# Optimization experiments

Measured on AMD Instinct MI355X. Metric: run time of the kernel, lower is better.

## Reference

```python
import jax, jax.numpy as jnp
import numpy as np

N = 100000   # nodes
E = 1600000  # edges (avg degree 16)
H = 4        # heads
D = 32       # per-head dim (= output_dim)
IN = 32      # input_dim (== output_dim for residual)
NEG_SLOPE = 0.2  # DGL GATConv leaky_relu default


def setup_inputs() -> dict:
    key = jax.random.key(0)
    ks = jax.random.split(key, 9)
    h = jax.random.normal(ks[0], (N, IN), jnp.float32)
    src = jax.random.randint(ks[1], (E,), 0, N, jnp.int32)
    dst = jax.random.randint(ks[2], (E,), 0, N, jnp.int32)
    W_fc = jax.random.normal(ks[3], (IN, H * D), jnp.float32) / np.sqrt(IN).astype(np.float32)
    attn_l = jax.random.normal(ks[4], (H, D), jnp.float32) * 0.1
    attn_r = jax.random.normal(ks[5], (H, D), jnp.float32) * 0.1
    bias_gat = jnp.zeros((H * D,), jnp.float32)
    W_out = jax.random.normal(ks[6], (H * D, D), jnp.float32) / np.sqrt(H * D).astype(np.float32)
    b_out = jnp.zeros((D,), jnp.float32)
    return {"h": h, "src": src, "dst": dst, "W_fc": W_fc, "attn_l": attn_l,
            "attn_r": attn_r, "bias_gat": bias_gat, "W_out": W_out, "b_out": b_out}


def reference(h, src, dst, W_fc, attn_l, attn_r, bias_gat, W_out, b_out):
    # GATConv: linear projection to [N, H, D]
    feat = (h @ W_fc).reshape(N, H, D)
    el = jnp.einsum('nhd,hd->nh', feat, attn_l)  # [N,H]
    er = jnp.einsum('nhd,hd->nh', feat, attn_r)  # [N,H]
    # per-edge unnormalized score, leaky relu
    e = el[src] + er[dst]                         # [E,H]
    e = jnp.where(e > 0, e, NEG_SLOPE * e)
    # segment softmax over edges grouped by destination node
    emax = jax.ops.segment_max(e, dst, num_segments=N)            # [N,H]
    ex = jnp.exp(e - emax[dst])                                   # [E,H]
    denom = jax.ops.segment_sum(ex, dst, num_segments=N)         # [N,H]
    alpha = ex / jnp.maximum(denom[dst], 1e-9)                    # [E,H]
    # attention-weighted scatter-add aggregation
    msg = feat[src] * alpha[:, :, None]                           # [E,H,D]
    rst = jax.ops.segment_sum(msg, dst, num_segments=N)          # [N,H,D]
    rst = rst.reshape(N, H * D) + bias_gat
    # out projection + ELU activation + residual
    out = rst @ W_out + b_out
    out = jnp.where(out > 0, out, jnp.expm1(out))  # ELU(alpha=1)
    return h + out
```

## Files before the change

### kernel.cpp

```cpp
#include <hip/hip_runtime.h>
#include <hip/hip_bf16.h>

#define NNODE 100000
#define NEDGE 1600000
#define NBLK_SCAN 98
#define KPH_BLOCKS 1564
#define FLAGBIT 0x80000000u

static __device__ __forceinline__ uint32_t pack_bf16(float a, float b) {
    __hip_bfloat162 t = __float22bfloat162_rn(make_float2(a, b));
    return *(uint32_t*)&t;
}

__global__ __launch_bounds__(256) void k_proj_hist(
        const float* __restrict__ hin, const float* __restrict__ Wfc,
        const float* __restrict__ attn_l, const float* __restrict__ attn_r,
        uint32_t* __restrict__ feat, float* __restrict__ el, float* __restrict__ er,
        const int* __restrict__ dst, int* __restrict__ cnt, int* __restrict__ pos) {
    int tid = threadIdx.x;
    int ei = blockIdx.x * 256 + tid;
    bool have = ei < NEDGE / 4;
    int4 d, p;
    if (have) {
        d = ((const int4*)dst)[ei];
        p.x = atomicAdd(&cnt[d.x], 1);
        p.y = atomicAdd(&cnt[d.y], 1);
        p.z = atomicAdd(&cnt[d.z], 1);
        p.w = atomicAdd(&cnt[d.w], 1);
    }
    int l = tid & 63;
    int w = tid >> 6;
    int nbase = blockIdx.x * 64 + w * 16;
    int c0 = l * 2;
    float2 wreg[32];
#pragma unroll
    for (int k = 0; k < 32; k++)
        wreg[k] = *(const float2*)&Wfc[k * 128 + c0];
    float al0 = attn_l[c0], al1 = attn_l[c0 + 1];
    float ar0 = attn_r[c0], ar1 = attn_r[c0 + 1];
#pragma unroll 4
    for (int i = 0; i < 16; i++) {
        int n = nbase + i;
        if (n >= NNODE) break;
        float4 hv[8];
#pragma unroll
        for (int j = 0; j < 8; j++)
            hv[j] = *(const float4*)&hin[n * 32 + j * 4];
        float a0 = 0.f, a1 = 0.f;
#pragma unroll
        for (int j = 0; j < 8; j++) {
            a0 = fmaf(hv[j].x, wreg[j * 4 + 0].x, a0); a1 = fmaf(hv[j].x, wreg[j * 4 + 0].y, a1);
            a0 = fmaf(hv[j].y, wreg[j * 4 + 1].x, a0); a1 = fmaf(hv[j].y, wreg[j * 4 + 1].y, a1);
            a0 = fmaf(hv[j].z, wreg[j * 4 + 2].x, a0); a1 = fmaf(hv[j].z, wreg[j * 4 + 2].y, a1);
            a0 = fmaf(hv[j].w, wreg[j * 4 + 3].x, a0); a1 = fmaf(hv[j].w, wreg[j * 4 + 3].y, a1);
        }
        float ep = a0 * al0 + a1 * al1;
        float rp = a0 * ar0 + a1 * ar1;
#pragma unroll
        for (int m = 8; m; m >>= 1) {
            ep += __shfl_xor(ep, m);
            rp += __shfl_xor(rp, m);
        }
        if ((l & 15) == 0) {
            el[n * 4 + (l >> 4)] = ep;
            er[n * 4 + (l >> 4)] = rp;
        }
        feat[(size_t)n * 64 + l] = pack_bf16(a0, a1);
    }
    if (have) ((int4*)pos)[ei] = p;
}

__global__ __launch_bounds__(256) void k_scan(
        const int* __restrict__ cnt, unsigned* __restrict__ word,
        int* __restrict__ offa) {
    __shared__ int s[256];
    __shared__ int sBase;
    int t = threadIdx.x;
    int b = blockIdx.x;
    int base = b * 1024 + t * 4;
    int v[4];
#pragma unroll
    for (int i = 0; i < 4; i++) {
        int n = base + i;
        v[i] = (n < NNODE) ? cnt[n] : 0;
    }
    int sum = v[0] + v[1] + v[2] + v[3];
    s[t] = sum;
    __syncthreads();
    for (int d = 1; d < 256; d <<= 1) {
        int x = (t >= d) ? s[t - d] : 0;
        __syncthreads();
        s[t] += x;
        __syncthreads();
    }
    int excl = s[t] - sum;
    if (t == 255)
        __hip_atomic_store(&word[b], (unsigned)s[255] | FLAGBIT,
                           __ATOMIC_RELEASE, __HIP_MEMORY_SCOPE_AGENT);
    if (t < 64) {
        unsigned acc = 0;
        for (int i = t; i < b; i += 64) {
            unsigned wv;
            do {
                wv = __hip_atomic_load(&word[i], __ATOMIC_ACQUIRE, __HIP_MEMORY_SCOPE_AGENT);
            } while (!(wv & FLAGBIT));
            acc += wv & ~FLAGBIT;
        }
#pragma unroll
        for (int o = 32; o; o >>= 1) acc += __shfl_down(acc, o);
        if (t == 0) sBase = (int)acc;
    }
    __syncthreads();
    int o0 = sBase + excl;
#pragma unroll
    for (int i = 0; i < 4; i++) {
        int n = base + i;
        if (n < NNODE) { offa[n] = o0; o0 += v[i]; }
    }
    if (b == NBLK_SCAN - 1 && t == 255) offa[NNODE] = NEDGE;
}

__global__ __launch_bounds__(256) void k_scatter(const int* __restrict__ src,
                                                 const int* __restrict__ dst,
                                                 const int* __restrict__ pos,
                                                 const int* __restrict__ offa,
                                                 int* __restrict__ ssrc) {
    int i = blockIdx.x * 256 + threadIdx.x;
    if (i >= NEDGE / 4) return;
    int4 s = ((const int4*)src)[i];
    int4 d = ((const int4*)dst)[i];
    int4 p = ((const int4*)pos)[i];
    int o0 = offa[d.x];
    int o1 = offa[d.y];
    int o2 = offa[d.z];
    int o3 = offa[d.w];
    ssrc[o0 + p.x] = s.x;
    ssrc[o1 + p.y] = s.y;
    ssrc[o2 + p.z] = s.z;
    ssrc[o3 + p.w] = s.w;
}

#define NPB 4
union SmemU {
    struct { int sS[NPB][64]; float sE[NPB][64][4]; } g;
    struct { float sv[NPB][128]; float sacc[NPB][2][32]; } e;
};

__global__ __launch_bounds__(256) void k_gather(
        const int* __restrict__ off, const int* __restrict__ ssrc,
        const float* __restrict__ el, const float* __restrict__ er,
        const uint32_t* __restrict__ feat, const float* __restrict__ bias_gat,
        const float* __restrict__ Wout, const float* __restrict__ b_out,
        const float* __restrict__ hin, float* __restrict__ out) {
    __shared__ float sW[128 * 32];
    __shared__ __align__(16) SmemU U;
    int tid = threadIdx.x;
    for (int i = tid * 4; i < 4096; i += 1024)
        *(float4*)&sW[i] = *(const float4*)&Wout[i];
    int w = tid >> 6;
    int l = tid & 63;
    int n = blockIdx.x * NPB + w;
    int c0 = l * 2;
    int hh = l >> 4;
    float2 acc = make_float2(0.f, 0.f);
    float den = 0.f;
    int beg = off[n], end = off[n + 1];
    float4 erv = *(const float4*)&er[n * 4];

    for (int base = beg; base < end; base += 64) {
        int cnt = end - base; if (cnt > 64) cnt = 64;
        int s = 0;
        float4 e4 = make_float4(0.f, 0.f, 0.f, 0.f);
        if (l < cnt) {
            s = ssrc[base + l];
            float4 ev = *(const float4*)&el[s * 4];
            e4.x = ev.x + erv.x; e4.x = e4.x > 0.f ? e4.x : 0.2f * e4.x; e4.x = __expf(e4.x);
            e4.y = ev.y + erv.y; e4.y = e4.y > 0.f ? e4.y : 0.2f * e4.y; e4.y = __expf(e4.y);
            e4.z = ev.z + erv.z; e4.z = e4.z > 0.f ? e4.z : 0.2f * e4.z; e4.z = __expf(e4.z);
            e4.w = ev.w + erv.w; e4.w = e4.w > 0.f ? e4.w : 0.2f * e4.w; e4.w = __expf(e4.w);
        }
        U.g.sS[w][l] = s;
        *(float4*)&U.g.sE[w][l][0] = e4;
        __builtin_amdgcn_wave_barrier();
        int rounds = (cnt + 7) >> 3;
        for (int r = 0; r < rounds; r++) {
            int e = r * 8;
            int ss[8]; float xx[8]; uint32_t uu[8];
#pragma unroll
            for (int q = 0; q < 8; q++) {
                ss[q] = U.g.sS[w][e + q];
                xx[q] = U.g.sE[w][e + q][hh];
            }
#pragma unroll
            for (int q = 0; q < 8; q++)
                uu[q] = feat[(uint32_t)ss[q] * 64u + (uint32_t)l];
#pragma unroll
            for (int q = 0; q < 8; q++) {
                den += xx[q];
                acc.x = fmaf(xx[q], __uint_as_float(uu[q] << 16), acc.x);
                acc.y = fmaf(xx[q], __uint_as_float(uu[q] & 0xffff0000u), acc.y);
            }
        }
        __builtin_amdgcn_wave_barrier();
    }
    float inv = 1.f / fmaxf(den, 1e-9f);
    float2 val;
    val.x = acc.x * inv + bias_gat[c0];
    val.y = acc.y * inv + bias_gat[c0 + 1];
    __syncthreads();
    *(float2*)&U.e.sv[w][c0] = val;
    __syncthreads();
    int j = tid & 31, g2 = (l >> 5);
    float p = 0.f;
    const float* vv = U.e.sv[w];
#pragma unroll 16
    for (int cc = g2 * 64; cc < g2 * 64 + 64; cc++)
        p = fmaf(vv[cc], sW[cc * 32 + j], p);
    U.e.sacc[w][g2][j] = p;
    __syncthreads();
    if (g2 == 0) {
        float a = U.e.sacc[w][0][j] + U.e.sacc[w][1][j] + b_out[j];
        a = a > 0.f ? a : expm1f(a);
        out[n * 32 + j] = hin[n * 32 + j] + a;
    }
}

extern "C" void kernel_launch(void* const* d_in, const int* in_sizes, int n_in,
                              void* d_out, int out_size, void* d_ws, size_t ws_size,
                              hipStream_t stream) {
    const float* hin      = (const float*)d_in[0];
    const int*   src      = (const int*)d_in[1];
    const int*   dst      = (const int*)d_in[2];
    const float* Wfc      = (const float*)d_in[3];
    const float* attn_l   = (const float*)d_in[4];
    const float* attn_r   = (const float*)d_in[5];
    const float* bias_gat = (const float*)d_in[6];
    const float* Wout     = (const float*)d_in[7];
    const float* b_out    = (const float*)d_in[8];
    float* out = (float*)d_out;

    char* ws = (char*)d_ws;
    size_t o = 0;
    uint32_t* feat = (uint32_t*)(ws + o); o += (size_t)NNODE * 64 * 4;
    float* el      = (float*)(ws + o);    o += (size_t)NNODE * 4 * 4;
    float* er      = (float*)(ws + o);    o += (size_t)NNODE * 4 * 4;
    int*   cnt     = (int*)(ws + o);      o += (size_t)NNODE * 4;
    unsigned* word = (unsigned*)(ws + o); o += (size_t)NBLK_SCAN * 4;
    int*   offa    = (int*)(ws + o);      o += (size_t)(NNODE + 1) * 4;
    int*   pos     = (int*)(ws + o);      o += (size_t)NEDGE * 4;
    int*   ssrc    = (int*)(ws + o);      o += (size_t)NEDGE * 4;

    hipMemsetAsync(cnt, 0, (size_t)(NNODE + NBLK_SCAN) * 4, stream);

    k_proj_hist<<<KPH_BLOCKS, 256, 0, stream>>>(
        hin, Wfc, attn_l, attn_r, feat, el, er, dst, cnt, pos);
    k_scan<<<NBLK_SCAN, 256, 0, stream>>>(cnt, word, offa);
    k_scatter<<<(NEDGE / 4 + 255) / 256, 256, 0, stream>>>(src, dst, pos, offa, ssrc);
    k_gather<<<NNODE / NPB, 256, 0, stream>>>(offa, ssrc, el, er, feat, bias_gat,
                                              Wout, b_out, hin, out);
}
```

Baseline: 224.3 us.

## Split degree histogram into four partitions and pack Wout to bf16 in shared memory

Result: no change. 222.6 us (-0.8%).

```diff
diff --git a/kernel.cpp b/kernel.cpp
--- a/kernel.cpp
+++ b/kernel.cpp
@@ -5,6 +5,7 @@
 #define NEDGE 1600000
 #define NBLK_SCAN 98
 #define KPH_BLOCKS 1564
+#define QINT4 100000
 #define FLAGBIT 0x80000000u
 
 static __device__ __forceinline__ uint32_t pack_bf16(float a, float b) {
@@ -21,12 +22,15 @@
     int ei = blockIdx.x * 256 + tid;
     bool have = ei < NEDGE / 4;
     int4 d, p;
+    int* cntp = nullptr;
     if (have) {
+        unsigned part = (unsigned)ei / (unsigned)QINT4;
+        cntp = cnt + part * NNODE;
         d = ((const int4*)dst)[ei];
-        p.x = atomicAdd(&cnt[d.x], 1);
-        p.y = atomicAdd(&cnt[d.y], 1);
-        p.z = atomicAdd(&cnt[d.z], 1);
-        p.w = atomicAdd(&cnt[d.w], 1);
+        p.x = atomicAdd(&cntp[d.x], 1);
+        p.y = atomicAdd(&cntp[d.y], 1);
+        p.z = atomicAdd(&cntp[d.z], 1);
+        p.w = atomicAdd(&cntp[d.w], 1);
     }
     int l = tid & 63;
     int w = tid >> 6;
@@ -72,17 +76,21 @@
 
 __global__ __launch_bounds__(256) void k_scan(
         const int* __restrict__ cnt, unsigned* __restrict__ word,
-        int* __restrict__ offa) {
+        int* __restrict__ offa, int* __restrict__ pb) {
     __shared__ int s[256];
     __shared__ int sBase;
     int t = threadIdx.x;
     int b = blockIdx.x;
     int base = b * 1024 + t * 4;
-    int v[4];
+    int vA[4], vB[4], vC[4], v[4];
 #pragma unroll
     for (int i = 0; i < 4; i++) {
         int n = base + i;
-        v[i] = (n < NNODE) ? cnt[n] : 0;
+        if (n < NNODE) {
+            int a = cnt[n], bb = cnt[NNODE + n], c = cnt[2 * NNODE + n], dd = cnt[3 * NNODE + n];
+            vA[i] = a; vB[i] = bb; vC[i] = c;
+            v[i] = a + bb + c + dd;
+        } else { vA[i] = vB[i] = vC[i] = 0; v[i] = 0; }
     }
     int sum = v[0] + v[1] + v[2] + v[3];
     s[t] = sum;
@@ -115,7 +123,14 @@
 #pragma unroll
     for (int i = 0; i < 4; i++) {
         int n = base + i;
-        if (n < NNODE) { offa[n] = o0; o0 += v[i]; }
+        if (n < NNODE) {
+            offa[n] = o0;
+            pb[n] = o0;
+            pb[NNODE + n] = o0 + vA[i];
+            pb[2 * NNODE + n] = o0 + vA[i] + vB[i];
+            pb[3 * NNODE + n] = o0 + vA[i] + vB[i] + vC[i];
+            o0 += v[i];
+        }
     }
     if (b == NBLK_SCAN - 1 && t == 255) offa[NNODE] = NEDGE;
 }
@@ -123,17 +138,19 @@
 __global__ __launch_bounds__(256) void k_scatter(const int* __restrict__ src,
                                                  const int* __restrict__ dst,
                                                  const int* __restrict__ pos,
-                                                 const int* __restrict__ offa,
+                                                 const int* __restrict__ pb,
                                                  int* __restrict__ ssrc) {
     int i = blockIdx.x * 256 + threadIdx.x;
     if (i >= NEDGE / 4) return;
+    unsigned part = (unsigned)i / (unsigned)QINT4;
+    const int* pbp = pb + part * NNODE;
     int4 s = ((const int4*)src)[i];
     int4 d = ((const int4*)dst)[i];
     int4 p = ((const int4*)pos)[i];
-    int o0 = offa[d.x];
-    int o1 = offa[d.y];
-    int o2 = offa[d.z];
-    int o3 = offa[d.w];
+    int o0 = pbp[d.x];
+    int o1 = pbp[d.y];
+    int o2 = pbp[d.z];
+    int o3 = pbp[d.w];
     ssrc[o0 + p.x] = s.x;
     ssrc[o1 + p.y] = s.y;
     ssrc[o2 + p.z] = s.z;
@@ -152,11 +169,13 @@
         const uint32_t* __restrict__ feat, const float* __restrict__ bias_gat,
         const float* __restrict__ Wout, const float* __restrict__ b_out,
         const float* __restrict__ hin, float* __restrict__ out) {
-    __shared__ float sW[128 * 32];
+    __shared__ uint32_t sWu[64 * 32];
     __shared__ __align__(16) SmemU U;
     int tid = threadIdx.x;
-    for (int i = tid * 4; i < 4096; i += 1024)
-        *(float4*)&sW[i] = *(const float4*)&Wout[i];
+    for (int i = tid; i < 2048; i += 256) {
+        int ccp = i >> 5, j = i & 31;
+        sWu[i] = pack_bf16(Wout[(2 * ccp) * 32 + j], Wout[(2 * ccp + 1) * 32 + j]);
+    }
     int w = tid >> 6;
     int l = tid & 63;
     int n = blockIdx.x * NPB + w;
@@ -213,9 +232,12 @@
     int j = tid & 31, g2 = (l >> 5);
     float p = 0.f;
     const float* vv = U.e.sv[w];
-#pragma unroll 16
-    for (int cc = g2 * 64; cc < g2 * 64 + 64; cc++)
-        p = fmaf(vv[cc], sW[cc * 32 + j], p);
+#pragma unroll 8
+    for (int ccp = g2 * 32; ccp < g2 * 32 + 32; ccp++) {
+        uint32_t u = sWu[ccp * 32 + j];
+        p = fmaf(vv[2 * ccp],     __uint_as_float(u << 16),          p);
+        p = fmaf(vv[2 * ccp + 1], __uint_as_float(u & 0xffff0000u), p);
+    }
     U.e.sacc[w][g2][j] = p;
     __syncthreads();
     if (g2 == 0) {
@@ -244,18 +266,19 @@
     uint32_t* feat = (uint32_t*)(ws + o); o += (size_t)NNODE * 64 * 4;
     float* el      = (float*)(ws + o);    o += (size_t)NNODE * 4 * 4;
     float* er      = (float*)(ws + o);    o += (size_t)NNODE * 4 * 4;
-    int*   cnt     = (int*)(ws + o);      o += (size_t)NNODE * 4;
+    int*   cnt     = (int*)(ws + o);      o += (size_t)4 * NNODE * 4;
     unsigned* word = (unsigned*)(ws + o); o += (size_t)NBLK_SCAN * 4;
     int*   offa    = (int*)(ws + o);      o += (size_t)(NNODE + 1) * 4;
+    int*   pb      = (int*)(ws + o);      o += (size_t)4 * NNODE * 4;
     int*   pos     = (int*)(ws + o);      o += (size_t)NEDGE * 4;
     int*   ssrc    = (int*)(ws + o);      o += (size_t)NEDGE * 4;
 
-    hipMemsetAsync(cnt, 0, (size_t)(NNODE + NBLK_SCAN) * 4, stream);
+    hipMemsetAsync(cnt, 0, (size_t)(4 * NNODE + NBLK_SCAN) * 4, stream);
 
     k_proj_hist<<<KPH_BLOCKS, 256, 0, stream>>>(
         hin, Wfc, attn_l, attn_r, feat, el, er, dst, cnt, pos);
-    k_scan<<<NBLK_SCAN, 256, 0, stream>>>(cnt, word, offa);
-    k_scatter<<<(NEDGE / 4 + 255) / 256, 256, 0, stream>>>(src, dst, pos, offa, ssrc);
+    k_scan<<<NBLK_SCAN, 256, 0, stream>>>(cnt, word, offa, pb);
+    k_scatter<<<(NEDGE / 4 + 255) / 256, 256, 0, stream>>>(src, dst, pos, pb, ssrc);
     k_gather<<<NNODE / NPB, 256, 0, stream>>>(offa, ssrc, el, er, feat, bias_gat,
                                               Wout, b_out, hin, out);
 }
```
